# Performance work log

Measured on AMD Instinct MI355X. Metric: run time of the kernel, lower is better.

Reference implementation:

```python
import jax, jax.numpy as jnp
import numpy as np

D = 64      # deg_dim
T = 3       # num_deg_types

def setup_inputs() -> dict:
    key = jax.random.key(0)
    ks = jax.random.split(key, 7)
    B, H, W = 4, 256, 256
    s = lambda *sh: 1.0 / np.sqrt(sh[0])
    inp = {
        "deg_features": jax.random.normal(ks[0], (B, T * D, H, W), dtype=jnp.float32),
        # graph_att: Linear(2D -> D), GELU, Linear(D -> 1), Sigmoid
        "W1": jax.random.normal(ks[1], (2 * D, D), dtype=jnp.float32) * s(2 * D),
        "b1": jax.random.normal(ks[2], (D,), dtype=jnp.float32) * 0.01,
        "W2": jax.random.normal(ks[3], (D, 1), dtype=jnp.float32) * s(D),
        "b2": jax.random.normal(ks[4], (1,), dtype=jnp.float32) * 0.01,
        # fusion: 1x1 Conv2d(T*D -> D), expressed as (T*D, D) matrix
        "Wf": jax.random.normal(ks[5], (T * D, D), dtype=jnp.float32) * s(T * D),
        "bf": jax.random.normal(ks[6], (D,), dtype=jnp.float32) * 0.01,
    }
    return inp

def reference(deg_features, W1, b1, W2, b2, Wf, bf):
    B, C, H, W = deg_features.shape
    # split channel into T blocks of D, move channels last: (B, T, H, W, D)
    x = deg_features.reshape(B, T, D, H, W).transpose(0, 1, 3, 4, 2)
    # Linear on concat([x_i, x_j]) decomposes: concat @ W1 = x_i @ W1[:D] + x_j @ W1[D:]
    a = jnp.einsum('bthwd,de->bthwe', x, W1[:D])   # contribution of i-feature
    c = jnp.einsum('bthwd,de->bthwe', x, W1[D:])   # contribution of j-feature
    outs = []
    for i in range(T):
        acc = x[:, i]  # diagonal weight is 1
        for j in range(T):
            if i == j:
                continue
            h = jax.nn.gelu(a[:, i] + c[:, j] + b1, approximate=False)  # (B,H,W,D)
            w = jax.nn.sigmoid(h @ W2 + b2)                             # (B,H,W,1)
            acc = acc + w * x[:, j]
        outs.append(acc)
    cat = jnp.stack(outs, axis=3)                  # (B,H,W,T,D)
    flat = cat.reshape(B, H, W, T * D)
    out = flat @ Wf + bf                           # 1x1 conv as matmul
    return out.transpose(0, 3, 1, 2)               # (B, D, H, W)
```

## Files before the change

kernel.cpp:

```cpp
#include <hip/hip_runtime.h>

#define HW 65536

typedef __attribute__((ext_vector_type(8))) short short8;
typedef __attribute__((ext_vector_type(4))) float f32x4;

static __device__ __forceinline__ unsigned short f2bf(float f) {
    unsigned int u = __float_as_uint(f);
    u += 0x7FFFu + ((u >> 16) & 1u);
    return (unsigned short)(u >> 16);
}
static __device__ __forceinline__ float bf2f(unsigned short s) {
    return __uint_as_float(((unsigned int)s) << 16);
}

__global__ void dig_prep(const float* __restrict__ W1, const float* __restrict__ Wf,
                         unsigned short* __restrict__ w1t, unsigned short* __restrict__ wft) {
    int tid = blockIdx.x * blockDim.x + threadIdx.x;
    int stride = gridDim.x * blockDim.x;
    for (int i = tid; i < 128 * 64; i += stride) {
        int r = i >> 6, d = i & 63;
        int kind = r >> 6, e = r & 63;
        w1t[i] = f2bf(W1[(kind * 64 + d) * 64 + e]);
    }
    for (int i = tid; i < 64 * 192; i += stride) {
        int r = i / 192, c = i - r * 192;
        wft[i] = f2bf(Wf[c * 64 + r]);
    }
}

__global__ __launch_bounds__(256, 4) void dig_main(
    const float* __restrict__ x,
    const float* __restrict__ W1,
    const float* __restrict__ b1,
    const float* __restrict__ W2,
    const float* __restrict__ b2,
    const float* __restrict__ Wf,
    const float* __restrict__ bfv,
    float* __restrict__ out,
    const unsigned short* __restrict__ w1t_g,
    const unsigned short* __restrict__ wft_g,
    int wsok)
{
    __shared__ __align__(16) unsigned short XS[32 * 200];
    __shared__ __align__(16) unsigned short ACC[32 * 200];
    __shared__ float GT[192];
    __shared__ float BW[132];

    const int tid = threadIdx.x;
    const int l   = tid & 63;
    const int w   = tid >> 6;
    const int lm  = l & 15;
    const int q   = l >> 4;

    const int tile = blockIdx.x;
    const int bb   = tile >> 11;
    const int hw0  = (tile & 2047) * 32;

    const float* xbase = x + (size_t)bb * (192 * HW) + hw0;
    for (int idx = tid; idx < 1536; idx += 256) {
        int c = idx >> 3, pg = idx & 7;
        float4 v = *(const float4*)(xbase + (size_t)c * HW + pg * 4);
        int p0 = pg * 4;
        XS[(p0 + 0) * 200 + c] = f2bf(v.x);
        XS[(p0 + 1) * 200 + c] = f2bf(v.y);
        XS[(p0 + 2) * 200 + c] = f2bf(v.z);
        XS[(p0 + 3) * 200 + c] = f2bf(v.w);
    }
    if (tid < 192)       GT[tid] = 0.f;
    if (tid < 64)        BW[tid] = b1[tid];
    else if (tid < 128)  BW[tid] = W2[tid - 64];
    else if (tid == 128) BW[128] = b2[0];
    __syncthreads();

    short8 afr[2][2];
    if (wsok) {
        #pragma unroll
        for (int kind = 0; kind < 2; ++kind)
            #pragma unroll
            for (int ks = 0; ks < 2; ++ks)
                afr[kind][ks] = *(const short8*)&w1t_g[(kind * 64 + w * 16 + lm) * 64 + ks * 32 + q * 8];
    } else {
        #pragma unroll
        for (int kind = 0; kind < 2; ++kind)
            #pragma unroll
            for (int ks = 0; ks < 2; ++ks) {
                union { short8 v; unsigned short u[8]; } tmp;
                #pragma unroll
                for (int j = 0; j < 8; ++j)
                    tmp.u[j] = f2bf(W1[(kind * 64 + ks * 32 + q * 8 + j) * 64 + (w * 16 + lm)]);
                afr[kind][ks] = tmp.v;
            }
    }

    f32x4 acc[2][3][2];
    #pragma unroll
    for (int kind = 0; kind < 2; ++kind)
        #pragma unroll
        for (int t = 0; t < 3; ++t)
            #pragma unroll
            for (int pt = 0; pt < 2; ++pt)
                acc[kind][t][pt] = (f32x4){0.f, 0.f, 0.f, 0.f};

    #pragma unroll
    for (int t = 0; t < 3; ++t) {
        short8 bfr[2][2];
        #pragma unroll
        for (int pt = 0; pt < 2; ++pt)
            #pragma unroll
            for (int ks = 0; ks < 2; ++ks)
                bfr[pt][ks] = *(const short8*)&XS[(pt * 16 + lm) * 200 + t * 64 + ks * 32 + q * 8];
        #pragma unroll
        for (int kind = 0; kind < 2; ++kind)
            #pragma unroll
            for (int pt = 0; pt < 2; ++pt) {
                acc[kind][t][pt] = __builtin_amdgcn_mfma_f32_16x16x32_bf16(
                    afr[kind][0], bfr[pt][0], acc[kind][t][pt], 0, 0, 0);
                acc[kind][t][pt] = __builtin_amdgcn_mfma_f32_16x16x32_bf16(
                    afr[kind][1], bfr[pt][1], acc[kind][t][pt], 0, 0, 0);
            }
    }

    {
        float4 b1v4 = *(const float4*)&BW[w * 16 + q * 4];
        float4 w2v4 = *(const float4*)&BW[64 + w * 16 + q * 4];
        const float b1a[4] = {b1v4.x, b1v4.y, b1v4.z, b1v4.w};
        const float w2a[4] = {w2v4.x, w2v4.y, w2v4.z, w2v4.w};
        #pragma unroll
        for (int pr = 0; pr < 6; ++pr) {
            const int i   = pr >> 1;
            const int j0c = (i == 0) ? 1 : 0;
            const int j1c = (i == 2) ? 1 : 2;
            const int j   = (pr & 1) ? j1c : j0c;
            #pragma unroll
            for (int pt = 0; pt < 2; ++pt) {
                float p = 0.f;
                #pragma unroll
                for (int r = 0; r < 4; ++r) {
                    float h  = acc[0][i][pt][r] + acc[1][j][pt][r] + b1a[r];
                    float h2 = h * h;
                    float u  = 0.7978845608f * __builtin_fmaf(0.044715f * h2, h, h);
                    float ex = __expf(2.0f * u);
                    float th = 1.0f - 2.0f / (ex + 1.0f);
                    float ge = 0.5f * h * (1.0f + th);
                    p = __builtin_fmaf(w2a[r], ge, p);
                }
                p += __shfl_xor(p, 16);
                p += __shfl_xor(p, 32);
                if (l < 16) atomicAdd(&GT[pr * 32 + pt * 16 + lm], p);
            }
        }
    }
    __syncthreads();

    {
        const int pix = tid >> 3;
        const int cg  = tid & 7;
        const float b2v = BW[128];
        const unsigned short* xrow = XS + pix * 200;
        unsigned short* arow = ACC + pix * 200;
        #pragma unroll
        for (int i = 0; i < 3; ++i) {
            const int j0c = (i == 0) ? 1 : 0;
            const int j1c = (i == 2) ? 1 : 2;
            float g0 = 1.0f / (1.0f + __expf(-(GT[(2 * i + 0) * 32 + pix] + b2v)));
            float g1 = 1.0f / (1.0f + __expf(-(GT[(2 * i + 1) * 32 + pix] + b2v)));
            #pragma unroll
            for (int ch = 0; ch < 2; ++ch) {
                int d0 = cg * 4 + ch * 32;
                ushort4 xi  = *(const ushort4*)&xrow[i * 64 + d0];
                ushort4 xj0 = *(const ushort4*)&xrow[j0c * 64 + d0];
                ushort4 xj1 = *(const ushort4*)&xrow[j1c * 64 + d0];
                ushort4 o;
                o.x = f2bf(bf2f(xi.x) + g0 * bf2f(xj0.x) + g1 * bf2f(xj1.x));
                o.y = f2bf(bf2f(xi.y) + g0 * bf2f(xj0.y) + g1 * bf2f(xj1.y));
                o.z = f2bf(bf2f(xi.z) + g0 * bf2f(xj0.z) + g1 * bf2f(xj1.z));
                o.w = f2bf(bf2f(xi.w) + g0 * bf2f(xj0.w) + g1 * bf2f(xj1.w));
                *(ushort4*)&arow[i * 64 + d0] = o;
            }
        }
    }
    __syncthreads();

    {
        const int mt  = w >> 1;
        const int ntb = (w & 1) * 2;
        f32x4 eacc[2];
        eacc[0] = (f32x4){0.f, 0.f, 0.f, 0.f};
        eacc[1] = (f32x4){0.f, 0.f, 0.f, 0.f};
        #pragma unroll
        for (int ks = 0; ks < 6; ++ks) {
            short8 af = *(const short8*)&ACC[(mt * 16 + lm) * 200 + ks * 32 + q * 8];
            #pragma unroll
            for (int ntl = 0; ntl < 2; ++ntl) {
                short8 bw8;
                if (wsok) {
                    bw8 = *(const short8*)&wft_g[((ntb + ntl) * 16 + lm) * 192 + ks * 32 + q * 8];
                } else {
                    union { short8 v; unsigned short u[8]; } tmp;
                    #pragma unroll
                    for (int j = 0; j < 8; ++j)
                        tmp.u[j] = f2bf(Wf[(ks * 32 + q * 8 + j) * 64 + (ntb + ntl) * 16 + lm]);
                    bw8 = tmp.v;
                }
                eacc[ntl] = __builtin_amdgcn_mfma_f32_16x16x32_bf16(af, bw8, eacc[ntl], 0, 0, 0);
            }
        }
        #pragma unroll
        for (int ntl = 0; ntl < 2; ++ntl) {
            int o = (ntb + ntl) * 16 + lm;
            float bo = bfv[o];
            float* obase = out + (size_t)bb * (64 * HW) + (size_t)o * HW + hw0 + mt * 16 + q * 4;
            *(float4*)obase = make_float4(eacc[ntl][0] + bo, eacc[ntl][1] + bo,
                                          eacc[ntl][2] + bo, eacc[ntl][3] + bo);
        }
    }
}

extern "C" void kernel_launch(void* const* d_in, const int* in_sizes, int n_in,
                              void* d_out, int out_size, void* d_ws, size_t ws_size,
                              hipStream_t stream) {
    (void)in_sizes; (void)n_in; (void)out_size;
    const float* x  = (const float*)d_in[0];
    const float* W1 = (const float*)d_in[1];
    const float* b1 = (const float*)d_in[2];
    const float* W2 = (const float*)d_in[3];
    const float* b2 = (const float*)d_in[4];
    const float* Wf = (const float*)d_in[5];
    const float* bf = (const float*)d_in[6];
    float* out = (float*)d_out;

    unsigned short* w1t = (unsigned short*)d_ws;
    unsigned short* wft = w1t + 128 * 64;
    const size_t need = (size_t)(128 * 64 + 64 * 192) * sizeof(unsigned short);
    int wsok = (d_ws != nullptr && ws_size >= need) ? 1 : 0;

    if (wsok) dig_prep<<<dim3(80), dim3(256), 0, stream>>>(W1, Wf, w1t, wft);
    dig_main<<<dim3(8192), dim3(256), 0, stream>>>(x, W1, b1, W2, b2, Wf, bf, out,
                                                   w1t, wft, wsok);
}
```

Baseline: 368.4 us.

## Cut registers and LDS, fast GELU, in-place mixing, raise occupancy

The first GEMM is split per pixel tile so only half the accumulators are live at once. The GELU epilogue now uses a sigmoid-form tanh approximation with exp2 and rcp intrinsics, and the gate sigmoid uses the same fast path. The separate ACC shared buffer is removed: each thread loads its x row into registers first, then writes the mixed result back into XS in place. Launch bounds rise from 4 to 6 waves per SIMD to exploit the lower LDS and register use. The risks are register spills under the tighter bound and slightly different GELU rounding.

```diff
diff --git a/kernel.cpp b/kernel.cpp
--- a/kernel.cpp
+++ b/kernel.cpp
@@ -12,6 +12,17 @@
 }
 static __device__ __forceinline__ float bf2f(unsigned short s) {
     return __uint_as_float(((unsigned int)s) << 16);
+}
+
+static __device__ __forceinline__ float gelu_sig(float h) {
+    float h2 = h * h;
+    float z  = h * __builtin_fmaf(-0.1029392f, h2, -2.3021178f);
+    float ex = __builtin_amdgcn_exp2f(z);
+    return h * __builtin_amdgcn_rcpf(1.0f + ex);
+}
+static __device__ __forceinline__ float sigmoid_fast(float v) {
+    float ex = __builtin_amdgcn_exp2f(-1.4426950f * v);
+    return __builtin_amdgcn_rcpf(1.0f + ex);
 }
 
 __global__ void dig_prep(const float* __restrict__ W1, const float* __restrict__ Wf,
@@ -29,7 +40,7 @@
     }
 }
 
-__global__ __launch_bounds__(256, 4) void dig_main(
+__global__ __launch_bounds__(256, 6) void dig_main(
     const float* __restrict__ x,
     const float* __restrict__ W1,
     const float* __restrict__ b1,
@@ -43,7 +54,6 @@
     int wsok)
 {
     __shared__ __align__(16) unsigned short XS[32 * 200];
-    __shared__ __align__(16) unsigned short ACC[32 * 200];
     __shared__ float GT[192];
     __shared__ float BW[132];
 
@@ -93,61 +103,53 @@
             }
     }
 
-    f32x4 acc[2][3][2];
-    #pragma unroll
-    for (int kind = 0; kind < 2; ++kind)
-        #pragma unroll
-        for (int t = 0; t < 3; ++t)
-            #pragma unroll
-            for (int pt = 0; pt < 2; ++pt)
-                acc[kind][t][pt] = (f32x4){0.f, 0.f, 0.f, 0.f};
-
-    #pragma unroll
-    for (int t = 0; t < 3; ++t) {
-        short8 bfr[2][2];
-        #pragma unroll
-        for (int pt = 0; pt < 2; ++pt)
-            #pragma unroll
-            for (int ks = 0; ks < 2; ++ks)
-                bfr[pt][ks] = *(const short8*)&XS[(pt * 16 + lm) * 200 + t * 64 + ks * 32 + q * 8];
-        #pragma unroll
-        for (int kind = 0; kind < 2; ++kind)
-            #pragma unroll
-            for (int pt = 0; pt < 2; ++pt) {
-                acc[kind][t][pt] = __builtin_amdgcn_mfma_f32_16x16x32_bf16(
-                    afr[kind][0], bfr[pt][0], acc[kind][t][pt], 0, 0, 0);
-                acc[kind][t][pt] = __builtin_amdgcn_mfma_f32_16x16x32_bf16(
-                    afr[kind][1], bfr[pt][1], acc[kind][t][pt], 0, 0, 0);
-            }
-    }
-
     {
         float4 b1v4 = *(const float4*)&BW[w * 16 + q * 4];
         float4 w2v4 = *(const float4*)&BW[64 + w * 16 + q * 4];
         const float b1a[4] = {b1v4.x, b1v4.y, b1v4.z, b1v4.w};
         const float w2a[4] = {w2v4.x, w2v4.y, w2v4.z, w2v4.w};
-        #pragma unroll
-        for (int pr = 0; pr < 6; ++pr) {
-            const int i   = pr >> 1;
-            const int j0c = (i == 0) ? 1 : 0;
-            const int j1c = (i == 2) ? 1 : 2;
-            const int j   = (pr & 1) ? j1c : j0c;
-            #pragma unroll
-            for (int pt = 0; pt < 2; ++pt) {
-                float p = 0.f;
-                #pragma unroll
-                for (int r = 0; r < 4; ++r) {
-                    float h  = acc[0][i][pt][r] + acc[1][j][pt][r] + b1a[r];
-                    float h2 = h * h;
-                    float u  = 0.7978845608f * __builtin_fmaf(0.044715f * h2, h, h);
-                    float ex = __expf(2.0f * u);
-                    float th = 1.0f - 2.0f / (ex + 1.0f);
-                    float ge = 0.5f * h * (1.0f + th);
-                    p = __builtin_fmaf(w2a[r], ge, p);
+
+        #pragma unroll
+        for (int pt = 0; pt < 2; ++pt) {
+            f32x4 acc[2][3];
+            #pragma unroll
+            for (int kind = 0; kind < 2; ++kind)
+                #pragma unroll
+                for (int t = 0; t < 3; ++t)
+                    acc[kind][t] = (f32x4){0.f, 0.f, 0.f, 0.f};
+
+            #pragma unroll
+            for (int t = 0; t < 3; ++t) {
+                const unsigned short* xr = &XS[(pt * 16 + lm) * 200 + t * 64 + q * 8];
+                short8 bfr0 = *(const short8*)xr;
+                short8 bfr1 = *(const short8*)(xr + 32);
+                #pragma unroll
+                for (int kind = 0; kind < 2; ++kind) {
+                    acc[kind][t] = __builtin_amdgcn_mfma_f32_16x16x32_bf16(
+                        afr[kind][0], bfr0, acc[kind][t], 0, 0, 0);
+                    acc[kind][t] = __builtin_amdgcn_mfma_f32_16x16x32_bf16(
+                        afr[kind][1], bfr1, acc[kind][t], 0, 0, 0);
                 }
-                p += __shfl_xor(p, 16);
-                p += __shfl_xor(p, 32);
-                if (l < 16) atomicAdd(&GT[pr * 32 + pt * 16 + lm], p);
+            }
+
+            #pragma unroll
+            for (int i = 0; i < 3; ++i) {
+                float ab[4];
+                #pragma unroll
+                for (int r = 0; r < 4; ++r) ab[r] = acc[0][i][r] + b1a[r];
+                #pragma unroll
+                for (int jj = 0; jj < 2; ++jj) {
+                    const int j = (jj == 0) ? ((i == 0) ? 1 : 0) : ((i == 2) ? 1 : 2);
+                    float p = 0.f;
+                    #pragma unroll
+                    for (int r = 0; r < 4; ++r) {
+                        float h = ab[r] + acc[1][j][r];
+                        p = __builtin_fmaf(w2a[r], gelu_sig(h), p);
+                    }
+                    p += __shfl_xor(p, 16);
+                    p += __shfl_xor(p, 32);
+                    if (l < 16) atomicAdd(&GT[(2 * i + jj) * 32 + pt * 16 + lm], p);
+                }
             }
         }
     }
@@ -156,27 +158,46 @@
     {
         const int pix = tid >> 3;
         const int cg  = tid & 7;
+        unsigned short* xrow = XS + pix * 200;
+
+        ushort4 xv[3][2];
+        #pragma unroll
+        for (int t = 0; t < 3; ++t)
+            #pragma unroll
+            for (int ch = 0; ch < 2; ++ch)
+                xv[t][ch] = *(const ushort4*)&xrow[t * 64 + cg * 4 + ch * 32];
+
+        float fx[3][2][4];
+        #pragma unroll
+        for (int t = 0; t < 3; ++t)
+            #pragma unroll
+            for (int ch = 0; ch < 2; ++ch) {
+                fx[t][ch][0] = bf2f(xv[t][ch].x);
+                fx[t][ch][1] = bf2f(xv[t][ch].y);
+                fx[t][ch][2] = bf2f(xv[t][ch].z);
+                fx[t][ch][3] = bf2f(xv[t][ch].w);
+            }
+
         const float b2v = BW[128];
-        const unsigned short* xrow = XS + pix * 200;
-        unsigned short* arow = ACC + pix * 200;
+        float g[6];
+        #pragma unroll
+        for (int p6 = 0; p6 < 6; ++p6)
+            g[p6] = sigmoid_fast(GT[p6 * 32 + pix] + b2v);
+
         #pragma unroll
         for (int i = 0; i < 3; ++i) {
             const int j0c = (i == 0) ? 1 : 0;
             const int j1c = (i == 2) ? 1 : 2;
-            float g0 = 1.0f / (1.0f + __expf(-(GT[(2 * i + 0) * 32 + pix] + b2v)));
-            float g1 = 1.0f / (1.0f + __expf(-(GT[(2 * i + 1) * 32 + pix] + b2v)));
+            const float g0 = g[2 * i + 0];
+            const float g1 = g[2 * i + 1];
             #pragma unroll
             for (int ch = 0; ch < 2; ++ch) {
-                int d0 = cg * 4 + ch * 32;
-                ushort4 xi  = *(const ushort4*)&xrow[i * 64 + d0];
-                ushort4 xj0 = *(const ushort4*)&xrow[j0c * 64 + d0];
-                ushort4 xj1 = *(const ushort4*)&xrow[j1c * 64 + d0];
                 ushort4 o;
-                o.x = f2bf(bf2f(xi.x) + g0 * bf2f(xj0.x) + g1 * bf2f(xj1.x));
-                o.y = f2bf(bf2f(xi.y) + g0 * bf2f(xj0.y) + g1 * bf2f(xj1.y));
-                o.z = f2bf(bf2f(xi.z) + g0 * bf2f(xj0.z) + g1 * bf2f(xj1.z));
-                o.w = f2bf(bf2f(xi.w) + g0 * bf2f(xj0.w) + g1 * bf2f(xj1.w));
-                *(ushort4*)&arow[i * 64 + d0] = o;
+                o.x = f2bf(__builtin_fmaf(g1, fx[j1c][ch][0], __builtin_fmaf(g0, fx[j0c][ch][0], fx[i][ch][0])));
+                o.y = f2bf(__builtin_fmaf(g1, fx[j1c][ch][1], __builtin_fmaf(g0, fx[j0c][ch][1], fx[i][ch][1])));
+                o.z = f2bf(__builtin_fmaf(g1, fx[j1c][ch][2], __builtin_fmaf(g0, fx[j0c][ch][2], fx[i][ch][2])));
+                o.w = f2bf(__builtin_fmaf(g1, fx[j1c][ch][3], __builtin_fmaf(g0, fx[j0c][ch][3], fx[i][ch][3])));
+                *(ushort4*)&xrow[i * 64 + cg * 4 + ch * 32] = o;
             }
         }
     }
@@ -190,7 +211,7 @@
         eacc[1] = (f32x4){0.f, 0.f, 0.f, 0.f};
         #pragma unroll
         for (int ks = 0; ks < 6; ++ks) {
-            short8 af = *(const short8*)&ACC[(mt * 16 + lm) * 200 + ks * 32 + q * 8];
+            short8 af = *(const short8*)&XS[(mt * 16 + lm) * 200 + ks * 32 + q * 8];
             #pragma unroll
             for (int ntl = 0; ntl < 2; ++ntl) {
                 short8 bw8;
```

After: 352.0 us. 1.05x faster.
